# Kernel optimization log

Measured on AMD Instinct MI355X. Metric: run time of the kernel, lower is better.

## Reference

```python
import jax, jax.numpy as jnp
import numpy as np

B, S, D, H, DK, DV, DFF, V, L = 2, 1024, 768, 12, 64, 64, 3072, 32000, 4
PAD_ID = 0


def _pos_enc(seq_len, dim):
    # sinusoidal PE: pe[:,0::2]=sin(pos/scale), pe[:,1::2]=cos(pos/scale)
    pos = jnp.arange(seq_len, dtype=jnp.float32)[:, None]
    idx = jnp.arange(dim // 2, dtype=jnp.float32)
    scale = 10000.0 ** (2.0 * idx / dim)
    ang = pos / scale  # [S, D/2]
    return jnp.stack([jnp.sin(ang), jnp.cos(ang)], axis=-1).reshape(seq_len, dim)


def _layernorm(x, s, b):
    m = jnp.mean(x, axis=-1, keepdims=True)
    v = jnp.var(x, axis=-1, keepdims=True)
    return (x - m) / jnp.sqrt(v + 1e-5) * s + b


def setup_inputs() -> dict:
    key = jax.random.key(0)
    ks = jax.random.split(key, 12)
    emb = jax.random.normal(ks[0], (V, D), jnp.float32) * 0.02
    emb = emb.at[PAD_ID].set(0.0)  # padding_idx row zeroed (nn.Embedding padding_idx)
    inp = {
        'x': jax.random.randint(ks[1], (B, S), 0, V),
        'emb': emb,
        'Wq': jax.random.normal(ks[2], (L, D, H * DK), jnp.float32) * 0.02,
        'Wk': jax.random.normal(ks[3], (L, D, H * DK), jnp.float32) * 0.02,
        'Wv': jax.random.normal(ks[4], (L, D, H * DV), jnp.float32) * 0.02,
        'Wo': jax.random.normal(ks[5], (L, H * DV, D), jnp.float32) * 0.02,
        'ln1_s': jnp.ones((L, D), jnp.float32),
        'ln1_b': jnp.zeros((L, D), jnp.float32),
        'W1': jax.random.normal(ks[6], (L, D, DFF), jnp.float32) * 0.02,
        'b1': jnp.zeros((L, DFF), jnp.float32),
        'W2': jax.random.normal(ks[7], (L, DFF, D), jnp.float32) * 0.02,
        'b2': jnp.zeros((L, D), jnp.float32),
        'ln2_s': jnp.ones((L, D), jnp.float32),
        'ln2_b': jnp.zeros((L, D), jnp.float32),
        'lm_W': jax.random.normal(ks[8], (D, V), jnp.float32) * 0.02,
        'lm_b': jnp.zeros((V,), jnp.float32),
    }
    return inp


def reference(x, emb, Wq, Wk, Wv, Wo, ln1_s, ln1_b, W1, b1, W2, b2, ln2_s, ln2_b, lm_W, lm_b):
    Bx, Sx = x.shape
    h = emb[x] + _pos_enc(Sx, D)  # [B, S, D]
    # causal mask from torch.triu(ones, diagonal=0): True on diagonal and above
    # (each token is prevented from attending to itself and future tokens)
    mask = jnp.triu(jnp.ones((Sx, Sx), dtype=bool))
    inv_sqrt_dk = 1.0 / jnp.sqrt(jnp.float32(DK))
    for l in range(L):
        q = (h @ Wq[l]).reshape(Bx, Sx, H, DK).transpose(0, 2, 1, 3)
        k = (h @ Wk[l]).reshape(Bx, Sx, H, DK).transpose(0, 2, 1, 3)
        v = (h @ Wv[l]).reshape(Bx, Sx, H, DV).transpose(0, 2, 1, 3)
        scores = jnp.einsum('bhqd,bhkd->bhqk', q, k) * inv_sqrt_dk
        scores = jnp.where(mask, -jnp.inf, scores)
        # source's custom _stable_softmax: exp(x) / (sum(exp(x)) + 1e-9)
        e = jnp.exp(scores)
        w = e / (jnp.sum(e, axis=-1, keepdims=True) + 1e-9)
        av = jnp.einsum('bhqk,bhkd->bhqd', w, v)
        av = av.transpose(0, 2, 1, 3).reshape(Bx, Sx, H * DV)
        h = _layernorm(h + av @ Wo[l], ln1_s[l], ln1_b[l])
        ff = jax.nn.gelu(h @ W1[l] + b1[l], approximate=False) @ W2[l] + b2[l]
        h = _layernorm(h + ff, ln2_s[l], ln2_b[l])
    return h @ lm_W + lm_b  # [B, S, V] logits
```

## Files before the change

### kernel.cpp

```cpp
#include <hip/hip_runtime.h>
#include <hip/hip_bf16.h>

#define L_LAYERS 4
#define D_MODEL 768
#define SEQ 1024
#define BATCH 2
#define NHEAD 12
#define HDIM 64
#define DFF_DIM 3072
#define VOCAB 32000
#define MROWS (BATCH*SEQ)
#define QKV_PLANE (NHEAD*BATCH*SEQ*HDIM)

typedef __attribute__((ext_vector_type(8))) short bfrag8;
typedef __attribute__((ext_vector_type(4))) float facc4;

#define EPI_PLAIN 0
#define EPI_BIAS 1
#define EPI_GELU_BF16 2
#define EPI_QKV 3

__device__ __forceinline__ void gld_lds16(const __hip_bfloat16* g, __hip_bfloat16* l) {
    __builtin_amdgcn_global_load_lds((const __attribute__((address_space(1))) void*)g,
                                     (__attribute__((address_space(3))) void*)l, 16, 0, 0);
}

__global__ __launch_bounds__(256) void transpose_cast(
    const float* __restrict__ src, __hip_bfloat16* __restrict__ dst,
    const int K, const int N, const long sL, const long dL)
{
    __shared__ float tile[32][33];
    const int z = blockIdx.z;
    const float* s = src + (long)z * sL;
    __hip_bfloat16* d = dst + (long)z * dL;
    const int bx = blockIdx.x * 32;
    const int by = blockIdx.y * 32;
    const int tx = threadIdx.x, ty = threadIdx.y;
    #pragma unroll
    for (int r = 0; r < 4; ++r)
        tile[ty + r*8][tx] = s[(long)(by + ty + r*8) * N + bx + tx];
    __syncthreads();
    #pragma unroll
    for (int r = 0; r < 4; ++r)
        d[(long)(bx + ty + r*8) * K + by + tx] = __float2bfloat16(tile[tx][ty + r*8]);
}

__global__ __launch_bounds__(256) void embed_k(
    const int* __restrict__ xids, const float* __restrict__ emb,
    float* __restrict__ h, __hip_bfloat16* __restrict__ hb)
{
    const int row = blockIdx.x, t = threadIdx.x;
    const int tok = xids[row];
    const int spos = row & (SEQ - 1);
    const long base = (long)row * D_MODEL;
    const long ebase = (long)tok * D_MODEL;
    #pragma unroll
    for (int j = 0; j < 3; ++j) {
        const int d = j*256 + t;
        const int i = d >> 1;
        const float ang = (float)spos * expf(-(float)(2*i) * (9.210340371976184f / 768.0f));
        const float pe = (d & 1) ? cosf(ang) : sinf(ang);
        const float v = emb[ebase + d] + pe;
        h[base + d] = v;
        hb[base + d] = __float2bfloat16(v);
    }
}

__global__ __launch_bounds__(256) void ln_residual(
    float* __restrict__ h, __hip_bfloat16* __restrict__ hb,
    const float* __restrict__ delta,
    const float* __restrict__ sc, const float* __restrict__ bi,
    const int nplanes)
{
    const int row = blockIdx.x, t = threadIdx.x;
    const long base = (long)row * D_MODEL;
    float x[3];
    float s1 = 0.f, s2 = 0.f;
    #pragma unroll
    for (int j = 0; j < 3; ++j) {
        const int d = j*256 + t;
        float v = h[base + d];
        for (int p = 0; p < nplanes; ++p)
            v += delta[(long)p * MROWS * D_MODEL + base + d];
        x[j] = v; s1 += v; s2 += v*v;
    }
    #pragma unroll
    for (int off = 32; off >= 1; off >>= 1) {
        s1 += __shfl_xor(s1, off);
        s2 += __shfl_xor(s2, off);
    }
    __shared__ float r1[4], r2[4];
    const int wv = t >> 6;
    if ((t & 63) == 0) { r1[wv] = s1; r2[wv] = s2; }
    __syncthreads();
    s1 = r1[0] + r1[1] + r1[2] + r1[3];
    s2 = r2[0] + r2[1] + r2[2] + r2[3];
    const float mean = s1 * (1.0f/768.0f);
    const float var  = s2 * (1.0f/768.0f) - mean*mean;
    const float inv  = rsqrtf(var + 1e-5f);
    #pragma unroll
    for (int j = 0; j < 3; ++j) {
        const int d = j*256 + t;
        const float y = (x[j] - mean) * inv * sc[d] + bi[d];
        h[base + d] = y;
        hb[base + d] = __float2bfloat16(y);
    }
}

__global__ __launch_bounds__(256) void gemm_bt(
    const __hip_bfloat16* __restrict__ A,
    const __hip_bfloat16* __restrict__ Bt,
    const float* __restrict__ bias,
    float* __restrict__ outf,
    __hip_bfloat16* __restrict__ outb,
    const int N, const int K, const int epi)
{
    __shared__ __hip_bfloat16 As[128*32];
    __shared__ __hip_bfloat16 Bs[128*32];
    const int tid = threadIdx.x;
    const int lane = tid & 63, wv = tid >> 6;

    const int nwg  = gridDim.x * gridDim.y;
    const int orig = blockIdx.y * gridDim.x + blockIdx.x;
    const int qq = nwg >> 3, rr = nwg & 7;
    const int xcd = orig & 7, lin = orig >> 3;
    const int wgid = (xcd < rr ? xcd * (qq + 1) : rr * (qq + 1) + (xcd - rr) * qq) + lin;
    const int bmi = wgid % gridDim.y;
    const int bni = wgid / gridDim.y;
    const int bm = bmi * 128, bn = bni * 128;

    const int wm = (wv >> 1) * 64, wn = (wv & 1) * 64;
    const int fr = lane & 15, fq = lane >> 4;

    const int Kc = K / gridDim.z;
    const long zoff = (long)blockIdx.z * Kc;

    facc4 acc[4][4];
    #pragma unroll
    for (int i = 0; i < 4; ++i)
        #pragma unroll
        for (int j = 0; j < 4; ++j) { facc4 z = {0.f,0.f,0.f,0.f}; acc[i][j] = z; }

    const int srow = wv*32 + (lane >> 2);
    const int scol = (lane & 3) * 8;
    const __hip_bfloat16* Ag = A  + (long)(bm + srow) * K + scol + zoff;
    const __hip_bfloat16* Bg = Bt + (long)(bn + srow) * K + scol + zoff;
    __hip_bfloat16* Asw = As + wv*1024;
    __hip_bfloat16* Bsw = Bs + wv*1024;

    for (int k0 = 0; k0 < Kc; k0 += 32) {
        __syncthreads();
        gld_lds16(Ag + k0,                 Asw);
        gld_lds16(Ag + k0 + (long)16*K,    Asw + 512);
        gld_lds16(Bg + k0,                 Bsw);
        gld_lds16(Bg + k0 + (long)16*K,    Bsw + 512);
        __syncthreads();
        bfrag8 af[4], bf[4];
        #pragma unroll
        for (int i = 0; i < 4; ++i) af[i] = *(const bfrag8*)(As + (wm + i*16 + fr)*32 + fq*8);
        #pragma unroll
        for (int j = 0; j < 4; ++j) bf[j] = *(const bfrag8*)(Bs + (wn + j*16 + fr)*32 + fq*8);
        #pragma unroll
        for (int i = 0; i < 4; ++i)
            #pragma unroll
            for (int j = 0; j < 4; ++j)
                acc[i][j] = __builtin_amdgcn_mfma_f32_16x16x32_bf16(af[i], bf[j], acc[i][j], 0, 0, 0);
    }

    if (epi == EPI_QKV) {
        __hip_bfloat16* qo = outb;
        __hip_bfloat16* ko = outb + QKV_PLANE;
        __hip_bfloat16* vo = outb + 2*QKV_PLANE;
        #pragma unroll
        for (int i = 0; i < 4; ++i) {
            #pragma unroll
            for (int j = 0; j < 4; ++j) {
                const int gn = bn + wn + j*16 + fr;
                const int which = gn / D_MODEL;
                const int nn = gn - which * D_MODEL;
                const int hh = nn >> 6, dd = nn & 63;
                #pragma unroll
                for (int r = 0; r < 4; ++r) {
                    const int gm = bm + wm + i*16 + fq*4 + r;
                    const int bidx = gm >> 10, si = gm & (SEQ-1);
                    const long bh = (long)bidx * NHEAD + hh;
                    const __hip_bfloat16 bv = __float2bfloat16(acc[i][j][r]);
                    if (which == 0)      qo[(bh*SEQ + si)*HDIM + dd] = bv;
                    else if (which == 1) ko[(bh*SEQ + si)*HDIM + dd] = bv;
                    else                 vo[(bh*HDIM + dd)*SEQ + si] = bv;
                }
            }
        }
    } else if (epi == EPI_GELU_BF16) {
        #pragma unroll
        for (int i = 0; i < 4; ++i)
            #pragma unroll
            for (int j = 0; j < 4; ++j) {
                const int gn = bn + wn + j*16 + fr;
                const float bb = bias[gn];
                #pragma unroll
                for (int r = 0; r < 4; ++r) {
                    const int gm = bm + wm + i*16 + fq*4 + r;
                    const float v = acc[i][j][r] + bb;
                    const float g = 0.5f * v * (1.0f + erff(v * 0.70710678118f));
                    outb[(long)gm * N + gn] = __float2bfloat16(g);
                }
            }
    } else if (epi == EPI_BIAS) {
        float* outz = outf + (long)blockIdx.z * (long)(gridDim.y * 128) * N;
        #pragma unroll
        for (int i = 0; i < 4; ++i)
            #pragma unroll
            for (int j = 0; j < 4; ++j) {
                const int gn = bn + wn + j*16 + fr;
                const float bb = (blockIdx.z == 0) ? bias[gn] : 0.f;
                #pragma unroll
                for (int r = 0; r < 4; ++r) {
                    const int gm = bm + wm + i*16 + fq*4 + r;
                    outz[(long)gm * N + gn] = acc[i][j][r] + bb;
                }
            }
    } else {
        float* outz = outf + (long)blockIdx.z * (long)(gridDim.y * 128) * N;
        #pragma unroll
        for (int i = 0; i < 4; ++i)
            #pragma unroll
            for (int j = 0; j < 4; ++j) {
                const int gn = bn + wn + j*16 + fr;
                #pragma unroll
                for (int r = 0; r < 4; ++r) {
                    const int gm = bm + wm + i*16 + fq*4 + r;
                    outz[(long)gm * N + gn] = acc[i][j][r];
                }
            }
    }
}

#define KS_STRIDE 80
#define VS_STRIDE 40
#define PS_STRIDE 40
__global__ __launch_bounds__(256) void attn_flash(
    const __hip_bfloat16* __restrict__ Q,
    const __hip_bfloat16* __restrict__ Kp,
    const __hip_bfloat16* __restrict__ Vt,
    __hip_bfloat16* __restrict__ avo)
{
    __shared__ __hip_bfloat16 Ks[32*KS_STRIDE];
    __shared__ __hip_bfloat16 Vs[64*VS_STRIDE];
    __shared__ __hip_bfloat16 Ps[4][16*PS_STRIDE];
    const int tid = threadIdx.x;
    const int lane = tid & 63, wv = tid >> 6;
    const int fr = lane & 15, fq = lane >> 4;
    const int q0 = blockIdx.x * 64;
    const int bh = blockIdx.y;
    const int qrow = q0 + wv*16;

    const __hip_bfloat16* qp = Q + ((long)bh*SEQ + qrow + fr)*HDIM + fq*8;
    const bfrag8 aq0 = *(const bfrag8*)(qp);
    const bfrag8 aq1 = *(const bfrag8*)(qp + 32);

    facc4 accv[4];
    #pragma unroll
    for (int n = 0; n < 4; ++n) { facc4 z = {0.f,0.f,0.f,0.f}; accv[n] = z; }
    float denom[4] = {0.f, 0.f, 0.f, 0.f};

    const __hip_bfloat16* kg = Kp + ((long)bh*SEQ + (tid>>3))*HDIM + (tid&7)*8;
    const __hip_bfloat16* vg = Vt + ((long)bh*HDIM + (tid>>2))*SEQ + (tid&3)*8;
    __hip_bfloat16* ksw = Ks + (tid>>3)*KS_STRIDE + (tid&7)*8;
    __hip_bfloat16* vsw = Vs + (tid>>2)*VS_STRIDE + (tid&3)*8;

    const int kend = q0 + 64;
    for (int k0 = 0; k0 < kend; k0 += 32) {
        __syncthreads();
        *(bfrag8*)ksw = *(const bfrag8*)(kg + (long)k0 * HDIM);
        *(bfrag8*)vsw = *(const bfrag8*)(vg + k0);
        __syncthreads();
        #pragma unroll
        for (int t = 0; t < 2; ++t) {
            const int koff = t*16;
            const bfrag8 bk0 = *(const bfrag8*)(Ks + (koff + fr)*KS_STRIDE + fq*8);
            const bfrag8 bk1 = *(const bfrag8*)(Ks + (koff + fr)*KS_STRIDE + 32 + fq*8);
            facc4 sc = {0.f,0.f,0.f,0.f};
            sc = __builtin_amdgcn_mfma_f32_16x16x32_bf16(aq0, bk0, sc, 0, 0, 0);
            sc = __builtin_amdgcn_mfma_f32_16x16x32_bf16(aq1, bk1, sc, 0, 0, 0);
            const int ki = k0 + koff + fr;
            #pragma unroll
            for (int r = 0; r < 4; ++r) {
                const int qi = qrow + fq*4 + r;
                const float e = (ki < qi) ? __expf(sc[r] * 0.125f) : 0.f;
                denom[r] += e;
                Ps[wv][(fq*4 + r)*PS_STRIDE + koff + fr] = __float2bfloat16(e);
            }
        }
        __syncthreads();
        const bfrag8 ap = *(const bfrag8*)(&Ps[wv][fr*PS_STRIDE + fq*8]);
        #pragma unroll
        for (int n = 0; n < 4; ++n) {
            const bfrag8 bv = *(const bfrag8*)(Vs + (n*16 + fr)*VS_STRIDE + fq*8);
            accv[n] = __builtin_amdgcn_mfma_f32_16x16x32_bf16(ap, bv, accv[n], 0, 0, 0);
        }
    }

    #pragma unroll
    for (int r = 0; r < 4; ++r) {
        #pragma unroll
        for (int off = 1; off < 16; off <<= 1) denom[r] += __shfl_xor(denom[r], off);
    }
    const int bidx = bh / NHEAD, hh = bh % NHEAD;
    #pragma unroll
    for (int n = 0; n < 4; ++n) {
        #pragma unroll
        for (int r = 0; r < 4; ++r) {
            const int qi = qrow + fq*4 + r;
            const int dd = n*16 + fr;
            const float o = accv[n][r] / (denom[r] + 1e-9f);
            avo[((long)(bidx*SEQ + qi))*D_MODEL + hh*HDIM + dd] = __float2bfloat16(o);
        }
    }
}

extern "C" void kernel_launch(void* const* d_in, const int* in_sizes, int n_in,
                              void* d_out, int out_size, void* d_ws, size_t ws_size,
                              hipStream_t stream) {
    const int*   x    = (const int*)d_in[0];
    const float* emb  = (const float*)d_in[1];
    const float* Wq   = (const float*)d_in[2];
    const float* Wk   = (const float*)d_in[3];
    const float* Wv   = (const float*)d_in[4];
    const float* Wo   = (const float*)d_in[5];
    const float* ln1s = (const float*)d_in[6];
    const float* ln1b = (const float*)d_in[7];
    const float* W1   = (const float*)d_in[8];
    const float* b1   = (const float*)d_in[9];
    const float* W2   = (const float*)d_in[10];
    const float* b2   = (const float*)d_in[11];
    const float* ln2s = (const float*)d_in[12];
    const float* ln2b = (const float*)d_in[13];
    const float* lmW  = (const float*)d_in[14];
    const float* lmb  = (const float*)d_in[15];
    float* out = (float*)d_out;

    char* wsp = (char*)d_ws;
    size_t off = 0;
    auto take = [&](size_t bytes) -> char* {
        char* p = wsp + off;
        off += (bytes + 255) & ~(size_t)255;
        return p;
    };
    __hip_bfloat16* wqkvT = (__hip_bfloat16*)take((size_t)L_LAYERS*2304*768*2);
    __hip_bfloat16* woT   = (__hip_bfloat16*)take((size_t)L_LAYERS*768*768*2);
    __hip_bfloat16* w1T   = (__hip_bfloat16*)take((size_t)L_LAYERS*3072*768*2);
    __hip_bfloat16* w2T   = (__hip_bfloat16*)take((size_t)L_LAYERS*768*3072*2);
    __hip_bfloat16* lmT   = (__hip_bfloat16*)take((size_t)VOCAB*768*2);
    float*          hbuf  = (float*)take((size_t)MROWS*D_MODEL*4);
    __hip_bfloat16* hb    = (__hip_bfloat16*)take((size_t)MROWS*D_MODEL*2);
    __hip_bfloat16* qkvb  = (__hip_bfloat16*)take((size_t)3*QKV_PLANE*2);
    __hip_bfloat16* avb   = (__hip_bfloat16*)take((size_t)MROWS*D_MODEL*2);
    __hip_bfloat16* ffb   = (__hip_bfloat16*)take((size_t)MROWS*DFF_DIM*2);
    float*          tmp   = (float*)take((size_t)2*MROWS*D_MODEL*4);

    dim3 tb(32, 8);
    transpose_cast<<<dim3(24,24,4), tb, 0, stream>>>(Wq, wqkvT,              768, 768, (long)768*768, (long)2304*768);
    transpose_cast<<<dim3(24,24,4), tb, 0, stream>>>(Wk, wqkvT + 768*768,    768, 768, (long)768*768, (long)2304*768);
    transpose_cast<<<dim3(24,24,4), tb, 0, stream>>>(Wv, wqkvT + 2*768*768,  768, 768, (long)768*768, (long)2304*768);
    transpose_cast<<<dim3(24,24,4), tb, 0, stream>>>(Wo, woT,                768, 768, (long)768*768, (long)768*768);
    transpose_cast<<<dim3(96,24,4), tb, 0, stream>>>(W1, w1T,                768, 3072, (long)768*3072, (long)3072*768);
    transpose_cast<<<dim3(24,96,4), tb, 0, stream>>>(W2, w2T,                3072, 768, (long)3072*768, (long)768*3072);
    transpose_cast<<<dim3(1000,24,1), tb, 0, stream>>>(lmW, lmT,             768, VOCAB, 0, 0);

    embed_k<<<MROWS, 256, 0, stream>>>(x, emb, hbuf, hb);

    for (int l = 0; l < L_LAYERS; ++l) {
        gemm_bt<<<dim3(18,16), 256, 0, stream>>>(hb, wqkvT + (size_t)l*2304*768, nullptr,
                                                 nullptr, qkvb, 2304, 768, EPI_QKV);
        attn_flash<<<dim3(16,24), 256, 0, stream>>>(qkvb, qkvb + QKV_PLANE, qkvb + 2*QKV_PLANE, avb);
        gemm_bt<<<dim3(6,16,2), 256, 0, stream>>>(avb, woT + (size_t)l*768*768, nullptr,
                                                  tmp, nullptr, 768, 768, EPI_PLAIN);
        ln_residual<<<MROWS, 256, 0, stream>>>(hbuf, hb, tmp, ln1s + l*768, ln1b + l*768, 2);
        gemm_bt<<<dim3(24,16), 256, 0, stream>>>(hb, w1T + (size_t)l*3072*768, b1 + l*DFF_DIM,
                                                 nullptr, ffb, DFF_DIM, 768, EPI_GELU_BF16);
        gemm_bt<<<dim3(6,16,2), 256, 0, stream>>>(ffb, w2T + (size_t)l*768*3072, b2 + l*768,
                                                  tmp, nullptr, 768, DFF_DIM, EPI_BIAS);
        ln_residual<<<MROWS, 256, 0, stream>>>(hbuf, hb, tmp, ln2s + l*768, ln2b + l*768, 2);
    }
    gemm_bt<<<dim3(250,16), 256, 0, stream>>>(hb, lmT, lmb, out, nullptr, VOCAB, 768, EPI_BIAS);
}
```

Baseline: 1.359 ms.

## Double-buffer GEMM LDS, prefetch attention K/V, remap tiles, split-K 4 for FFN2

The GEMM kernel now double-buffers its LDS tiles so the global-to-LDS load of the next K slice overlaps the MFMA work on the current one. It also remaps workgroup IDs so groups of 8 M-tiles share each N column, aiming for better L2 reuse. The attention kernel prefetches the next K/V chunk into registers and replaces a block barrier with a per-wave LDS waitcnt. It also raises wave priority around the MFMA sections. The FFN down-projection moves to 4-way split-K, which needs a larger partial-sum buffer and makes the LayerNorm sum four partials, adding extra memory traffic in exchange for more parallelism.

```diff
diff --git a/kernel.cpp b/kernel.cpp
--- a/kernel.cpp
+++ b/kernel.cpp
@@ -115,8 +115,8 @@
     __hip_bfloat16* __restrict__ outb,
     const int N, const int K, const int epi)
 {
-    __shared__ __hip_bfloat16 As[128*32];
-    __shared__ __hip_bfloat16 Bs[128*32];
+    __shared__ __hip_bfloat16 As[2][128*32];
+    __shared__ __hip_bfloat16 Bs[2][128*32];
     const int tid = threadIdx.x;
     const int lane = tid & 63, wv = tid >> 6;
 
@@ -125,8 +125,10 @@
     const int qq = nwg >> 3, rr = nwg & 7;
     const int xcd = orig & 7, lin = orig >> 3;
     const int wgid = (xcd < rr ? xcd * (qq + 1) : rr * (qq + 1) + (xcd - rr) * qq) + lin;
-    const int bmi = wgid % gridDim.y;
-    const int bni = wgid / gridDim.y;
+    const int m8   = wgid & 7;
+    const int rest = wgid >> 3;
+    const int bni  = rest % gridDim.x;
+    const int bmi  = (rest / gridDim.x) * 8 + m8;
     const int bm = bmi * 128, bn = bni * 128;
 
     const int wm = (wv >> 1) * 64, wn = (wv & 1) * 64;
@@ -145,26 +147,42 @@
     const int scol = (lane & 3) * 8;
     const __hip_bfloat16* Ag = A  + (long)(bm + srow) * K + scol + zoff;
     const __hip_bfloat16* Bg = Bt + (long)(bn + srow) * K + scol + zoff;
-    __hip_bfloat16* Asw = As + wv*1024;
-    __hip_bfloat16* Bsw = Bs + wv*1024;
-
-    for (int k0 = 0; k0 < Kc; k0 += 32) {
+    __hip_bfloat16* Aw0 = &As[0][wv*1024];
+    __hip_bfloat16* Aw1 = &As[1][wv*1024];
+    __hip_bfloat16* Bw0 = &Bs[0][wv*1024];
+    __hip_bfloat16* Bw1 = &Bs[1][wv*1024];
+
+    const int nt = Kc >> 5;
+    gld_lds16(Ag,                 Aw0);
+    gld_lds16(Ag + (long)16*K,    Aw0 + 512);
+    gld_lds16(Bg,                 Bw0);
+    gld_lds16(Bg + (long)16*K,    Bw0 + 512);
+
+    int cur = 0;
+    for (int t = 0; t < nt; ++t) {
         __syncthreads();
-        gld_lds16(Ag + k0,                 Asw);
-        gld_lds16(Ag + k0 + (long)16*K,    Asw + 512);
-        gld_lds16(Bg + k0,                 Bsw);
-        gld_lds16(Bg + k0 + (long)16*K,    Bsw + 512);
-        __syncthreads();
+        if (t + 1 < nt) {
+            const int k0 = (t + 1) << 5;
+            __hip_bfloat16* aw = cur ? Aw0 : Aw1;
+            __hip_bfloat16* bw = cur ? Bw0 : Bw1;
+            gld_lds16(Ag + k0,              aw);
+            gld_lds16(Ag + k0 + (long)16*K, aw + 512);
+            gld_lds16(Bg + k0,              bw);
+            gld_lds16(Bg + k0 + (long)16*K, bw + 512);
+        }
+        const __hip_bfloat16* Ab = cur ? &As[1][0] : &As[0][0];
+        const __hip_bfloat16* Bb = cur ? &Bs[1][0] : &Bs[0][0];
         bfrag8 af[4], bf[4];
         #pragma unroll
-        for (int i = 0; i < 4; ++i) af[i] = *(const bfrag8*)(As + (wm + i*16 + fr)*32 + fq*8);
-        #pragma unroll
-        for (int j = 0; j < 4; ++j) bf[j] = *(const bfrag8*)(Bs + (wn + j*16 + fr)*32 + fq*8);
+        for (int i = 0; i < 4; ++i) af[i] = *(const bfrag8*)(Ab + (wm + i*16 + fr)*32 + fq*8);
+        #pragma unroll
+        for (int j = 0; j < 4; ++j) bf[j] = *(const bfrag8*)(Bb + (wn + j*16 + fr)*32 + fq*8);
         #pragma unroll
         for (int i = 0; i < 4; ++i)
             #pragma unroll
             for (int j = 0; j < 4; ++j)
                 acc[i][j] = __builtin_amdgcn_mfma_f32_16x16x32_bf16(af[i], bf[j], acc[i][j], 0, 0, 0);
+        cur ^= 1;
     }
 
     if (epi == EPI_QKV) {
@@ -269,11 +287,17 @@
     __hip_bfloat16* ksw = Ks + (tid>>3)*KS_STRIDE + (tid&7)*8;
     __hip_bfloat16* vsw = Vs + (tid>>2)*VS_STRIDE + (tid&3)*8;
 
+    bfrag8 kr = *(const bfrag8*)(kg);
+    bfrag8 vr = *(const bfrag8*)(vg);
+
     const int kend = q0 + 64;
     for (int k0 = 0; k0 < kend; k0 += 32) {
         __syncthreads();
-        *(bfrag8*)ksw = *(const bfrag8*)(kg + (long)k0 * HDIM);
-        *(bfrag8*)vsw = *(const bfrag8*)(vg + k0);
+        *(bfrag8*)ksw = kr;
+        *(bfrag8*)vsw = vr;
+        const long knext = (k0 + 32 < kend) ? (long)(k0 + 32) : (long)k0;
+        kr = *(const bfrag8*)(kg + knext * HDIM);
+        vr = *(const bfrag8*)(vg + knext);
         __syncthreads();
         #pragma unroll
         for (int t = 0; t < 2; ++t) {
@@ -281,8 +305,10 @@
             const bfrag8 bk0 = *(const bfrag8*)(Ks + (koff + fr)*KS_STRIDE + fq*8);
             const bfrag8 bk1 = *(const bfrag8*)(Ks + (koff + fr)*KS_STRIDE + 32 + fq*8);
             facc4 sc = {0.f,0.f,0.f,0.f};
+            __builtin_amdgcn_s_setprio(1);
             sc = __builtin_amdgcn_mfma_f32_16x16x32_bf16(aq0, bk0, sc, 0, 0, 0);
             sc = __builtin_amdgcn_mfma_f32_16x16x32_bf16(aq1, bk1, sc, 0, 0, 0);
+            __builtin_amdgcn_s_setprio(0);
             const int ki = k0 + koff + fr;
             #pragma unroll
             for (int r = 0; r < 4; ++r) {
@@ -292,13 +318,16 @@
                 Ps[wv][(fq*4 + r)*PS_STRIDE + koff + fr] = __float2bfloat16(e);
             }
         }
-        __syncthreads();
+        asm volatile("s_waitcnt lgkmcnt(0)" ::: "memory");
+        __builtin_amdgcn_sched_barrier(0);
         const bfrag8 ap = *(const bfrag8*)(&Ps[wv][fr*PS_STRIDE + fq*8]);
+        __builtin_amdgcn_s_setprio(1);
         #pragma unroll
         for (int n = 0; n < 4; ++n) {
             const bfrag8 bv = *(const bfrag8*)(Vs + (n*16 + fr)*VS_STRIDE + fq*8);
             accv[n] = __builtin_amdgcn_mfma_f32_16x16x32_bf16(ap, bv, accv[n], 0, 0, 0);
         }
+        __builtin_amdgcn_s_setprio(0);
     }
 
     #pragma unroll
@@ -357,7 +386,7 @@
     __hip_bfloat16* qkvb  = (__hip_bfloat16*)take((size_t)3*QKV_PLANE*2);
     __hip_bfloat16* avb   = (__hip_bfloat16*)take((size_t)MROWS*D_MODEL*2);
     __hip_bfloat16* ffb   = (__hip_bfloat16*)take((size_t)MROWS*DFF_DIM*2);
-    float*          tmp   = (float*)take((size_t)2*MROWS*D_MODEL*4);
+    float*          tmp   = (float*)take((size_t)4*MROWS*D_MODEL*4);
 
     dim3 tb(32, 8);
     transpose_cast<<<dim3(24,24,4), tb, 0, stream>>>(Wq, wqkvT,              768, 768, (long)768*768, (long)2304*768);
@@ -379,9 +408,9 @@
         ln_residual<<<MROWS, 256, 0, stream>>>(hbuf, hb, tmp, ln1s + l*768, ln1b + l*768, 2);
         gemm_bt<<<dim3(24,16), 256, 0, stream>>>(hb, w1T + (size_t)l*3072*768, b1 + l*DFF_DIM,
                                                  nullptr, ffb, DFF_DIM, 768, EPI_GELU_BF16);
-        gemm_bt<<<dim3(6,16,2), 256, 0, stream>>>(ffb, w2T + (size_t)l*768*3072, b2 + l*768,
+        gemm_bt<<<dim3(6,16,4), 256, 0, stream>>>(ffb, w2T + (size_t)l*768*3072, b2 + l*768,
                                                   tmp, nullptr, 768, DFF_DIM, EPI_BIAS);
-        ln_residual<<<MROWS, 256, 0, stream>>>(hbuf, hb, tmp, ln2s + l*768, ln2b + l*768, 2);
+        ln_residual<<<MROWS, 256, 0, stream>>>(hbuf, hb, tmp, ln2s + l*768, ln2b + l*768, 4);
     }
     gemm_bt<<<dim3(250,16), 256, 0, stream>>>(hb, lmT, lmb, out, nullptr, VOCAB, 768, EPI_BIAS);
 }
```

Result: faster. 1.164 ms (-14.4%).
